# Kernel optimization log

Measured on AMD Instinct MI355X. Metric: run time of the kernel, lower is better.

Reference implementation:

```python
import jax, jax.numpy as jnp
import numpy as np

N_NODES = 100000


def gcn_conv(x, W, b, row, col, n_nodes):
    # PyG GCNConv: x' = D^{-1/2} (A + I) D^{-1/2} (x W) + b
    xw = x @ W  # [N, out]
    ones = jnp.ones(row.shape[0], dtype=x.dtype)
    deg = jnp.zeros((n_nodes,), dtype=x.dtype).at[col].add(ones) + 1.0  # +1 self-loop
    dinv = jax.lax.rsqrt(deg)
    norm = dinv[row] * dinv[col]  # per-edge normalization [E]
    msgs = xw[row] * norm[:, None]  # gather + scale [E, out]
    agg = jax.ops.segment_sum(msgs, col, num_segments=n_nodes)
    # self-loop contribution: norm = deg^{-1/2} * deg^{-1/2} = 1/deg
    agg = agg + xw * (1.0 / deg)[:, None]
    return agg + b


def setup_inputs() -> dict:
    key = jax.random.key(0)
    k1, k2, k3, k4 = jax.random.split(key, 4)
    x = jax.random.normal(k1, (N_NODES, 128), dtype=jnp.float32)
    edge_index = jax.random.randint(k2, (2, 1600000), 0, N_NODES, dtype=jnp.int64)
    W1 = jax.random.normal(k3, (128, 256), dtype=jnp.float32) * (1.0 / np.sqrt(128))
    b1 = jnp.zeros((256,), dtype=jnp.float32)
    W2 = jax.random.normal(k4, (256, 128), dtype=jnp.float32) * (1.0 / np.sqrt(256))
    b2 = jnp.zeros((128,), dtype=jnp.float32)
    return {"x": x, "edge_index": edge_index, "W1": W1, "b1": b1, "W2": W2, "b2": b2}


def reference(x, edge_index, W1, b1, W2, b2):
    row, col = edge_index[0], edge_index[1]
    n = x.shape[0]
    h = gcn_conv(x, W1, b1, row, col, n)
    h = jax.nn.gelu(h)
    out = gcn_conv(h, W2, b2, row, col, n)
    return out
```

## Files before the change

### kernel.cpp

```cpp
#include <hip/hip_runtime.h>
#include <hip/hip_bf16.h>
#include <math.h>

typedef __attribute__((ext_vector_type(8))) short bf16x8;
typedef __attribute__((ext_vector_type(4))) float f32x4;

__device__ inline ushort f2bf(float f) {
    uint u = __float_as_uint(f);
    uint r = u + 0x7fffu + ((u >> 16) & 1u);
    return (ushort)(r >> 16);
}
__device__ inline float bf2f(ushort h) { return __uint_as_float(((uint)h) << 16); }

__device__ inline float gelu_fast(float x) {
    float z2 = 1.5957691216057308f * (x + 0.044715f * x * x * x);
    return x / (1.0f + __expf(-z2));
}


__global__ void deg_rank_kernel(const int* __restrict__ col, int* __restrict__ deg,
                                int* __restrict__ rank, int E) {
    int e = blockIdx.x * blockDim.x + threadIdx.x;
    if (e < E) rank[e] = atomicAdd(&deg[col[e]], 1);
}

__global__ void dinv_kernel(const int* __restrict__ deg, float* __restrict__ dinv, int M) {
    int i = blockIdx.x * blockDim.x + threadIdx.x;
    if (i < M) dinv[i] = rsqrtf((float)deg[i] + 1.0f);
}


__global__ void block_reduce_kernel(const int* __restrict__ deg, int* __restrict__ bsum, int M) {
    __shared__ int s[256];
    int i = blockIdx.x * 256 + threadIdx.x;
    s[threadIdx.x] = (i < M) ? deg[i] : 0;
    __syncthreads();
    for (int o = 128; o > 0; o >>= 1) {
        if (threadIdx.x < o) s[threadIdx.x] += s[threadIdx.x + o];
        __syncthreads();
    }
    if (threadIdx.x == 0) bsum[blockIdx.x] = s[0];
}

__global__ void scan_bsum_kernel(int* __restrict__ bsum, int nb) {
    __shared__ int s[512];
    int t = threadIdx.x;
    int orig = (t < nb) ? bsum[t] : 0;
    s[t] = orig;
    __syncthreads();
    for (int o = 1; o < 512; o <<= 1) {
        int v = 0;
        if (t >= o) v = s[t - o];
        __syncthreads();
        if (t >= o) s[t] += v;
        __syncthreads();
    }
    if (t < nb) bsum[t] = s[t] - orig;
}

__global__ void scan_offsets_kernel(const int* __restrict__ deg, const int* __restrict__ bsum,
                                    int* __restrict__ off, int M) {
    __shared__ int s[256];
    int i = blockIdx.x * 256 + threadIdx.x;
    int orig = (i < M) ? deg[i] : 0;
    s[threadIdx.x] = orig;
    __syncthreads();
    for (int o = 1; o < 256; o <<= 1) {
        int v = 0;
        if (threadIdx.x >= o) v = s[threadIdx.x - o];
        __syncthreads();
        if (threadIdx.x >= o) s[threadIdx.x] += v;
        __syncthreads();
    }
    if (i < M) off[i] = bsum[blockIdx.x] + s[threadIdx.x] - orig;
}


__global__ void fill_sorted_kernel(const int* __restrict__ row, const int* __restrict__ col,
                                   const int* __restrict__ off, const int* __restrict__ rank,
                                   int* __restrict__ rs, int E) {
    int e = blockIdx.x * blockDim.x + threadIdx.x;
    if (e < E) rs[off[col[e]] + rank[e]] = row[e];
}


__global__ void prep_weights(const float* __restrict__ W1, const float* __restrict__ W2,
                             ushort* __restrict__ wt1h, ushort* __restrict__ wt1l,
                             ushort* __restrict__ wt2h, ushort* __restrict__ wt2l) {
    int idx = blockIdx.x * 256 + threadIdx.x;
    if (idx < 128 * 256) {
        int k = idx >> 8, n = idx & 255;
        float f = W1[idx];
        ushort h = f2bf(f);
        wt1h[n * 128 + k] = h;
        wt1l[n * 128 + k] = f2bf(f - bf2f(h));
    } else if (idx < 2 * 128 * 256) {
        int i2 = idx - 128 * 256;
        int k = i2 >> 7, n = i2 & 127;
        float f = W2[i2];
        ushort h = f2bf(f);
        wt2h[n * 256 + k] = h;
        wt2l[n * 256 + k] = f2bf(f - bf2f(h));
    }
}


__global__ void to_bf16_scaled_kernel(const float* __restrict__ in, const float* __restrict__ dinv,
                                      ushort* __restrict__ out, int n8) {
    int i = blockIdx.x * 256 + threadIdx.x;
    if (i >= n8) return;
    float s = dinv[i >> 4];
    float4 a = *(const float4*)(in + (size_t)i * 8);
    float4 b = *(const float4*)(in + (size_t)i * 8 + 4);
    ushort4 u0 = make_ushort4(f2bf(a.x * s), f2bf(a.y * s), f2bf(a.z * s), f2bf(a.w * s));
    ushort4 u1 = make_ushort4(f2bf(b.x * s), f2bf(b.y * s), f2bf(b.z * s), f2bf(b.w * s));
    *(ushort4*)(out + (size_t)i * 8) = u0;
    *(ushort4*)(out + (size_t)i * 8 + 4) = u1;
}


__global__ __launch_bounds__(256) void gemm_fused(const ushort* __restrict__ A,
                                                  const ushort* __restrict__ wt1h,
                                                  const ushort* __restrict__ wt1l,
                                                  const float* __restrict__ b1,
                                                  const ushort* __restrict__ wt2h,
                                                  const ushort* __restrict__ wt2l,
                                                  const float* __restrict__ dinv,
                                                  ushort* __restrict__ Cb, int M) {
    __shared__ ushort la[64 * 128];
    __shared__ ushort lh[64 * 256];

    const int t = threadIdx.x;
    const int R0 = blockIdx.x * 64;

    #pragma unroll
    for (int base = 0; base < 1024; base += 256) {
        int idx = base + t;
        int r = idx >> 4;
        int c8 = idx & 15;
        int gr = R0 + r;
        bf16x8 v = {};
        if (gr < M) v = *(const bf16x8*)(A + (size_t)gr * 128 + c8 * 8);
        int byte = (r * 128 + c8 * 8) * 2;
        byte ^= (r & 7) << 4;
        *(bf16x8*)((char*)la + byte) = v;
    }

    const int w = t >> 6, l = t & 63;
    const int lrow = l & 15;
    const int lk = l >> 4;

    bf16x8 w1h[4][4], w1l[4][4];
    {
        const int c0 = w * 64;
        #pragma unroll
        for (int n = 0; n < 4; ++n) {
            int oc = c0 + n * 16 + lrow;
            #pragma unroll
            for (int ks = 0; ks < 4; ++ks) {
                int kb = ks * 32 + lk * 8;
                w1h[n][ks] = *(const bf16x8*)&wt1h[(size_t)oc * 128 + kb];
                w1l[n][ks] = *(const bf16x8*)&wt1l[(size_t)oc * 128 + kb];
            }
        }
    }
    __syncthreads();

    {
        const int c0 = w * 64;
        f32x4 acc[4][4] = {};
        #pragma unroll
        for (int ks = 0; ks < 4; ++ks) {
            const int kb = ks * 32 + lk * 8;
            bf16x8 xf[4];
            #pragma unroll
            for (int m = 0; m < 4; ++m) {
                int nd = m * 16 + lrow;
                int byte = (nd * 128 + kb) * 2;
                byte ^= (nd & 7) << 4;
                xf[m] = *(const bf16x8*)((const char*)la + byte);
            }
            #pragma unroll
            for (int n = 0; n < 4; ++n)
                #pragma unroll
                for (int m = 0; m < 4; ++m) {
                    acc[n][m] = __builtin_amdgcn_mfma_f32_16x16x32_bf16(w1h[n][ks], xf[m], acc[n][m], 0, 0, 0);
                    acc[n][m] = __builtin_amdgcn_mfma_f32_16x16x32_bf16(w1l[n][ks], xf[m], acc[n][m], 0, 0, 0);
                }
        }
        #pragma unroll
        for (int n = 0; n < 4; ++n) {
            int ob = c0 + n * 16 + lk * 4;
            float4 bb = *(const float4*)(b1 + ob);
            #pragma unroll
            for (int m = 0; m < 4; ++m) {
                int nd = m * 16 + lrow;
                ushort4 pk;
                pk.x = f2bf(gelu_fast(acc[n][m][0] + bb.x));
                pk.y = f2bf(gelu_fast(acc[n][m][1] + bb.y));
                pk.z = f2bf(gelu_fast(acc[n][m][2] + bb.z));
                pk.w = f2bf(gelu_fast(acc[n][m][3] + bb.w));
                int byte = (nd * 256 + ob) * 2;
                byte ^= (nd & 7) << 4;
                *(ushort4*)((char*)lh + byte) = pk;
            }
        }
    }

    bf16x8 w2h[2][8], w2l[2][8];
    {
        const int c0 = w * 32;
        #pragma unroll
        for (int n = 0; n < 2; ++n) {
            int oc = c0 + n * 16 + lrow;
            #pragma unroll
            for (int ks = 0; ks < 8; ++ks) {
                int kb = ks * 32 + lk * 8;
                w2h[n][ks] = *(const bf16x8*)&wt2h[(size_t)oc * 256 + kb];
                w2l[n][ks] = *(const bf16x8*)&wt2l[(size_t)oc * 256 + kb];
            }
        }
    }
    __syncthreads();

    {
        const int c0 = w * 32;
        f32x4 acc2[2][4] = {};
        #pragma unroll
        for (int ks = 0; ks < 8; ++ks) {
            const int kb = ks * 32 + lk * 8;
            bf16x8 hf[4];
            #pragma unroll
            for (int m = 0; m < 4; ++m) {
                int nd = m * 16 + lrow;
                int byte = (nd * 256 + kb) * 2;
                byte ^= (nd & 7) << 4;
                hf[m] = *(const bf16x8*)((const char*)lh + byte);
            }
            #pragma unroll
            for (int n = 0; n < 2; ++n)
                #pragma unroll
                for (int m = 0; m < 4; ++m) {
                    acc2[n][m] = __builtin_amdgcn_mfma_f32_16x16x32_bf16(w2h[n][ks], hf[m], acc2[n][m], 0, 0, 0);
                    acc2[n][m] = __builtin_amdgcn_mfma_f32_16x16x32_bf16(w2l[n][ks], hf[m], acc2[n][m], 0, 0, 0);
                }
        }
        #pragma unroll
        for (int m = 0; m < 4; ++m) {
            int nd = m * 16 + lrow;
            int grow = R0 + nd;
            if (grow < M) {
                float sc = dinv[grow];
                #pragma unroll
                for (int n = 0; n < 2; ++n) {
                    int ob = c0 + n * 16 + lk * 4;
                    ushort4 pk;
                    pk.x = f2bf(acc2[n][m][0] * sc);
                    pk.y = f2bf(acc2[n][m][1] * sc);
                    pk.z = f2bf(acc2[n][m][2] * sc);
                    pk.w = f2bf(acc2[n][m][3] * sc);
                    *(ushort4*)(Cb + (size_t)grow * 128 + ob) = pk;
                }
            }
        }
    }
}


template <bool BIAS, bool OUTBF>
__global__ __launch_bounds__(256) void gather_sum_kernel(const int* __restrict__ off,
                                                         const int* __restrict__ deg,
                                                         const int* __restrict__ rs,
                                                         const float* __restrict__ dinv,
                                                         const ushort* __restrict__ srcb,
                                                         const float* __restrict__ b,
                                                         float* __restrict__ dstf,
                                                         ushort* __restrict__ dstb, int M) {
    int wid = (blockIdx.x * 256 + threadIdx.x) >> 6;
    int lane = threadIdx.x & 63;
    int grp = lane >> 4;
    int l16 = lane & 15;
    if (wid >= M) return;
    int s0 = off[wid];
    int n = deg[wid];
    float acc[8] = {};

    if (grp == 0) {
        bf16x8 u = *(const bf16x8*)(srcb + (size_t)wid * 128 + l16 * 8);
        #pragma unroll
        for (int i = 0; i < 8; ++i) acc[i] += bf2f((ushort)u[i]);
    }

    int j = 0;
    for (; j + 4 <= n; j += 4) {
        int r = rs[s0 + j + grp];
        bf16x8 u = *(const bf16x8*)(srcb + (size_t)r * 128 + l16 * 8);
        #pragma unroll
        for (int i = 0; i < 8; ++i) acc[i] += bf2f((ushort)u[i]);
    }
    if (j + grp < n) {
        int r = rs[s0 + j + grp];
        bf16x8 u = *(const bf16x8*)(srcb + (size_t)r * 128 + l16 * 8);
        #pragma unroll
        for (int i = 0; i < 8; ++i) acc[i] += bf2f((ushort)u[i]);
    }

    #pragma unroll
    for (int i = 0; i < 8; ++i) {
        acc[i] += __shfl_xor(acc[i], 16);
        acc[i] += __shfl_xor(acc[i], 32);
    }

    if (grp == 0) {
        float sc = dinv[wid];
        #pragma unroll
        for (int i = 0; i < 8; ++i) acc[i] *= sc;
        if constexpr (BIAS) {
            float4 b0 = *(const float4*)(b + l16 * 8);
            float4 b1v = *(const float4*)(b + l16 * 8 + 4);
            acc[0] += b0.x; acc[1] += b0.y; acc[2] += b0.z; acc[3] += b0.w;
            acc[4] += b1v.x; acc[5] += b1v.y; acc[6] += b1v.z; acc[7] += b1v.w;
        }
        if constexpr (OUTBF) {
            bf16x8 o;
            #pragma unroll
            for (int i = 0; i < 8; ++i) o[i] = (short)f2bf(acc[i]);
            *(bf16x8*)(dstb + (size_t)wid * 128 + l16 * 8) = o;
        } else {
            float4 o0 = make_float4(acc[0], acc[1], acc[2], acc[3]);
            float4 o1 = make_float4(acc[4], acc[5], acc[6], acc[7]);
            *(float4*)(dstf + (size_t)wid * 128 + l16 * 8) = o0;
            *(float4*)(dstf + (size_t)wid * 128 + l16 * 8 + 4) = o1;
        }
    }
}


extern "C" void kernel_launch(void* const* d_in, const int* in_sizes, int n_in,
                              void* d_out, int out_size, void* d_ws, size_t ws_size,
                              hipStream_t stream) {
    const float* x  = (const float*)d_in[0];
    const int*   ei = (const int*)d_in[1];
    const float* W1 = (const float*)d_in[2];
    const float* b1 = (const float*)d_in[3];
    const float* W2 = (const float*)d_in[4];
    const float* b2 = (const float*)d_in[5];

    const int M = in_sizes[0] / 128;
    const int E = in_sizes[1] / 2;
    const int* row = ei;
    const int* col = ei + E;

    ushort* xb    = (ushort*)d_ws;
    ushort* aggxb = xb + 12800000;
    ushort* xw2b  = aggxb;
    float*  dinv  = (float*)(aggxb + 12800000);
    int*    deg   = (int*)(dinv + 102400);
    int*    off   = deg + 102400;
    int*    rank  = off + 102400;
    int*    rs    = rank + 1600000;
    int*    bsum  = rs + 1600000;
    ushort* wt1h  = (ushort*)(bsum + 1024);
    ushort* wt1l  = wt1h + 32768;
    ushort* wt2h  = wt1l + 32768;
    ushort* wt2l  = wt2h + 32768;
    float*  outw  = (float*)d_out;

    const int nb = (M + 255) / 256;

    hipMemsetAsync(deg, 0, (size_t)102400 * sizeof(int), stream);

    deg_rank_kernel<<<(E + 255) / 256, 256, 0, stream>>>(col, deg, rank, E);
    dinv_kernel<<<(M + 255) / 256, 256, 0, stream>>>(deg, dinv, M);

    block_reduce_kernel<<<nb, 256, 0, stream>>>(deg, bsum, M);
    scan_bsum_kernel<<<1, 512, 0, stream>>>(bsum, nb);
    scan_offsets_kernel<<<nb, 256, 0, stream>>>(deg, bsum, off, M);

    fill_sorted_kernel<<<(E + 255) / 256, 256, 0, stream>>>(row, col, off, rank, rs, E);

    prep_weights<<<256, 256, 0, stream>>>(W1, W2, wt1h, wt1l, wt2h, wt2l);
    to_bf16_scaled_kernel<<<(M * 16 + 255) / 256, 256, 0, stream>>>(x, dinv, xb, M * 16);

    gather_sum_kernel<false, true><<<(M * 64 + 255) / 256, 256, 0, stream>>>(
        off, deg, rs, dinv, xb, nullptr, nullptr, aggxb, M);

    gemm_fused<<<(M + 63) / 64, 256, 0, stream>>>(aggxb, wt1h, wt1l, b1,
                                                  wt2h, wt2l, dinv, xw2b, M);

    gather_sum_kernel<true, false><<<(M * 64 + 255) / 256, 256, 0, stream>>>(
        off, deg, rs, dinv, xw2b, b2, outw, nullptr, M);
}
```

Baseline: 335.0 us.

## Load GEMM A operand directly from global and double-buffer gather accumulation

The fused GEMM no longer stages the 64x128 input tile into LDS. Each wave now reads its A fragments straight from global memory, which drops a shared buffer and a barrier, and launch bounds now request two blocks per CU. The gather-sum loop is unrolled to two independent neighbor loads per iteration with separate accumulators, so more memory requests are in flight. The risk is redundant global reads of A across the four waves, which may be uncoalesced per-lane 16-byte loads, plus higher register pressure.

```diff
diff --git a/kernel.cpp b/kernel.cpp
--- a/kernel.cpp
+++ b/kernel.cpp
@@ -119,33 +119,18 @@
 }
 
 
-__global__ __launch_bounds__(256) void gemm_fused(const ushort* __restrict__ A,
-                                                  const ushort* __restrict__ wt1h,
-                                                  const ushort* __restrict__ wt1l,
-                                                  const float* __restrict__ b1,
-                                                  const ushort* __restrict__ wt2h,
-                                                  const ushort* __restrict__ wt2l,
-                                                  const float* __restrict__ dinv,
-                                                  ushort* __restrict__ Cb, int M) {
-    __shared__ ushort la[64 * 128];
+__global__ __launch_bounds__(256, 2) void gemm_fused(const ushort* __restrict__ A,
+                                                     const ushort* __restrict__ wt1h,
+                                                     const ushort* __restrict__ wt1l,
+                                                     const float* __restrict__ b1,
+                                                     const ushort* __restrict__ wt2h,
+                                                     const ushort* __restrict__ wt2l,
+                                                     const float* __restrict__ dinv,
+                                                     ushort* __restrict__ Cb, int M) {
     __shared__ ushort lh[64 * 256];
 
     const int t = threadIdx.x;
     const int R0 = blockIdx.x * 64;
-
-    #pragma unroll
-    for (int base = 0; base < 1024; base += 256) {
-        int idx = base + t;
-        int r = idx >> 4;
-        int c8 = idx & 15;
-        int gr = R0 + r;
-        bf16x8 v = {};
-        if (gr < M) v = *(const bf16x8*)(A + (size_t)gr * 128 + c8 * 8);
-        int byte = (r * 128 + c8 * 8) * 2;
-        byte ^= (r & 7) << 4;
-        *(bf16x8*)((char*)la + byte) = v;
-    }
-
     const int w = t >> 6, l = t & 63;
     const int lrow = l & 15;
     const int lk = l >> 4;
@@ -164,7 +149,6 @@
             }
         }
     }
-    __syncthreads();
 
     {
         const int c0 = w * 64;
@@ -175,10 +159,9 @@
             bf16x8 xf[4];
             #pragma unroll
             for (int m = 0; m < 4; ++m) {
-                int nd = m * 16 + lrow;
-                int byte = (nd * 128 + kb) * 2;
-                byte ^= (nd & 7) << 4;
-                xf[m] = *(const bf16x8*)((const char*)la + byte);
+                int gr = R0 + m * 16 + lrow;
+                gr = gr < M ? gr : M - 1;
+                xf[m] = *(const bf16x8*)(A + (size_t)gr * 128 + kb);
             }
             #pragma unroll
             for (int n = 0; n < 4; ++n)
@@ -284,6 +267,7 @@
     int s0 = off[wid];
     int n = deg[wid];
     float acc[8] = {};
+    float acc2[8] = {};
 
     if (grp == 0) {
         bf16x8 u = *(const bf16x8*)(srcb + (size_t)wid * 128 + l16 * 8);
@@ -292,21 +276,34 @@
     }
 
     int j = 0;
-    for (; j + 4 <= n; j += 4) {
+    for (; j + 8 <= n; j += 8) {
+        int r0 = rs[s0 + j + grp];
+        int r1 = rs[s0 + j + 4 + grp];
+        bf16x8 u0 = *(const bf16x8*)(srcb + (size_t)r0 * 128 + l16 * 8);
+        bf16x8 u1 = *(const bf16x8*)(srcb + (size_t)r1 * 128 + l16 * 8);
+        #pragma unroll
+        for (int i = 0; i < 8; ++i) {
+            acc[i] += bf2f((ushort)u0[i]);
+            acc2[i] += bf2f((ushort)u1[i]);
+        }
+    }
+    if (j + 4 <= n) {
         int r = rs[s0 + j + grp];
         bf16x8 u = *(const bf16x8*)(srcb + (size_t)r * 128 + l16 * 8);
         #pragma unroll
         for (int i = 0; i < 8; ++i) acc[i] += bf2f((ushort)u[i]);
+        j += 4;
     }
     if (j + grp < n) {
         int r = rs[s0 + j + grp];
         bf16x8 u = *(const bf16x8*)(srcb + (size_t)r * 128 + l16 * 8);
         #pragma unroll
-        for (int i = 0; i < 8; ++i) acc[i] += bf2f((ushort)u[i]);
+        for (int i = 0; i < 8; ++i) acc2[i] += bf2f((ushort)u[i]);
     }
 
     #pragma unroll
     for (int i = 0; i < 8; ++i) {
+        acc[i] += acc2[i];
         acc[i] += __shfl_xor(acc[i], 16);
         acc[i] += __shfl_xor(acc[i], 32);
     }
```

After: 326.9 us. 2.4% less time.
